# Kernel tuning notes

Measured on AMD Instinct MI355X. Metric: run time of the kernel, lower is better.

Reference implementation:

```python
import jax, jax.numpy as jnp
import numpy as np

N, E, F, H, C, G = 100000, 800000, 128, 128, 10, 128
EPS = 1e-5


def setup_inputs() -> dict:
    key = jax.random.key(0)
    ks = jax.random.split(key, 8)
    return {
        "x": jax.random.normal(ks[0], (N, F), jnp.float32),
        "edge_index": jax.random.randint(ks[1], (2, E), 0, N),
        "batch": jnp.sort(jax.random.randint(ks[2], (N,), 0, G)),
        "edge_weight": jax.random.uniform(ks[3], (E,), jnp.float32, 0.1, 1.0),
        "bn_feat_w": jnp.ones((F,), jnp.float32),
        "bn_feat_b": jnp.full((F,), 1e-4, jnp.float32),
        "conv_feat_W": jax.random.normal(ks[4], (F, H), jnp.float32) / np.float32(np.sqrt(F)),
        "conv_feat_b": jnp.zeros((H,), jnp.float32),
        "bns_w": jnp.ones((3, H), jnp.float32),
        "bns_b": jnp.full((3, H), 1e-4, jnp.float32),
        "convs_W": jax.random.normal(ks[5], (3, H, H), jnp.float32) / np.float32(np.sqrt(H)),
        "convs_b": jnp.zeros((3, H), jnp.float32),
        "bn_fc_w": jnp.ones((H,), jnp.float32),
        "bn_fc_b": jnp.full((H,), 1e-4, jnp.float32),
        "lin_fc_W": jax.random.normal(ks[6], (H, H), jnp.float32) / np.float32(np.sqrt(H)),
        "lin_fc_b": jnp.zeros((H,), jnp.float32),
        "bn_hidden_w": jnp.ones((H,), jnp.float32),
        "bn_hidden_b": jnp.full((H,), 1e-4, jnp.float32),
        "lin_class_W": jax.random.normal(ks[7], (H, C), jnp.float32) / np.float32(np.sqrt(H)),
        "lin_class_b": jnp.zeros((C,), jnp.float32),
    }


def _bn(h, w, b):
    # training-mode BatchNorm1d: biased batch stats over dim 0
    mu = h.mean(0)
    var = jnp.mean((h - mu) ** 2, 0)
    return (h - mu) * jax.lax.rsqrt(var + EPS) * w + b


def reference(x, edge_index, batch, edge_weight,
              bn_feat_w, bn_feat_b, conv_feat_W, conv_feat_b,
              bns_w, bns_b, convs_W, convs_b,
              bn_fc_w, bn_fc_b, lin_fc_W, lin_fc_b,
              bn_hidden_w, bn_hidden_b, lin_class_W, lin_class_b):
    n = x.shape[0]
    loops = jnp.arange(n)
    # PyG GCNConv: add self-loops (weight 1) + symmetric normalization, shared by all convs
    row = jnp.concatenate([edge_index[0], loops])
    col = jnp.concatenate([edge_index[1], loops])
    ew = jnp.concatenate([edge_weight, jnp.ones((n,), x.dtype)])
    deg = jax.ops.segment_sum(ew, col, num_segments=n)
    dinv = jnp.where(deg > 0, jax.lax.rsqrt(jnp.maximum(deg, EPS)), 0.0)
    norm = (dinv[row] * ew * dinv[col])[:, None]  # [E+N, 1]

    def conv(h, W, b):
        m = (h @ W)[row] * norm                 # gather + scale per edge
        return jax.ops.segment_sum(m, col, num_segments=n) + b

    h = _bn(x, bn_feat_w, bn_feat_b)
    h = jax.nn.relu(conv(h, conv_feat_W, conv_feat_b))
    h_init = h

    x_list = []
    # branch 1: BN -> Conv -> ReLU chain
    h = h_init
    for i in range(3):
        h = jax.nn.relu(conv(_bn(h, bns_w[i], bns_b[i]), convs_W[i], convs_b[i]))
    x_list.append(h)
    # branch 2: double application of the same BN/Conv per step
    h = h_init
    for i in range(3):
        h_ = jax.nn.relu(conv(_bn(h, bns_w[i], bns_b[i]), convs_W[i], convs_b[i]))
        h = jax.nn.relu(conv(_bn(h_, bns_w[i], bns_b[i]), convs_W[i], convs_b[i]))
    x_list.append(h)
    # branch 3: identical to branch 1 when conv_residual=False
    h = h_init
    for i in range(3):
        h = jax.nn.relu(conv(_bn(h, bns_w[i], bns_b[i]), convs_W[i], convs_b[i]))
    x_list.append(h)
    # branch 4: BN -> ReLU only
    h = h_init
    for i in range(3):
        h = jax.nn.relu(_bn(h, bns_w[i], bns_b[i]))
    x_list.append(h)

    def head(hn):
        g = jax.ops.segment_sum(hn, batch, num_segments=G)  # global_add_pool
        g = jax.nn.relu(_bn(g, bn_fc_w, bn_fc_b) @ lin_fc_W + lin_fc_b)
        g = _bn(g, bn_hidden_w, bn_hidden_b)
        return jax.nn.log_softmax(g @ lin_class_W + lin_class_b, axis=-1)

    return tuple(head(hn) for hn in x_list)
```

## Files before the change

kernel.cpp:

```cpp
#include <hip/hip_runtime.h>

#define N_NODES 100000
#define NPAD    100032
#define NBLK    1563
#define NEDGE   800000
#define NGRP    128
#define NSLOT   32
#define EPS     1e-5f

typedef unsigned int   u32;
typedef unsigned short u16;
typedef short bf16x8 __attribute__((ext_vector_type(8)));
typedef float f32x4  __attribute__((ext_vector_type(4)));

__device__ __forceinline__ float bf2f(u32 u){ return __uint_as_float(u << 16); }
__device__ __forceinline__ u16 f2bf(float f){
  u32 x = __float_as_uint(f);
  x += 0x7fffu + ((x >> 16) & 1u);
  return (u16)(x >> 16);
}

__global__ void k_init(float* deg, int* cnt, int* fill, float* gbuf){
  int i = blockIdx.x * 256 + threadIdx.x;
  if (i < NPAD){ deg[i] = 1.0f; cnt[i] = 0; fill[i] = 0; }
  if (i < 4 * NGRP * 128) gbuf[i] = 0.f;
}

__global__ void k_deg(const int* __restrict__ col, const float* __restrict__ ew,
                      float* __restrict__ deg, int* __restrict__ cnt){
  int e = blockIdx.x * 256 + threadIdx.x;
  if (e < NEDGE){
    int c = col[e];
    atomicAdd(&deg[c], ew[e]);
    atomicAdd(&cnt[c], 1);
  }
}

__global__ void k_dinv(const float* __restrict__ deg, float* __restrict__ dinv, float* __restrict__ srow){
  int i = blockIdx.x * 256 + threadIdx.x;
  if (i < N_NODES){
    float d = deg[i];
    float v = d > 0.f ? rsqrtf(fmaxf(d, EPS)) : 0.f;
    dinv[i] = v; srow[i] = v * v;
  }
}

__global__ __launch_bounds__(256) void k_chunksum(const int* __restrict__ cnt, int* __restrict__ csum){
  int b = blockIdx.x, t = threadIdx.x;
  int s = 0;
  for (int i = t; i < 1024; i += 256){ int idx = b * 1024 + i; if (idx < N_NODES) s += cnt[idx]; }
  __shared__ int red[256];
  red[t] = s; __syncthreads();
  for (int o = 128; o > 0; o >>= 1){ if (t < o) red[t] += red[t + o]; __syncthreads(); }
  if (t == 0) csum[b] = red[0];
}

__global__ __launch_bounds__(128) void k_chunkscan(const int* __restrict__ csum, int* __restrict__ coff,
                                                   int* __restrict__ ptrA){
  int t = threadIdx.x;
  __shared__ int s[128];
  int v = (t < 98) ? csum[t] : 0;
  s[t] = v; __syncthreads();
  for (int o = 1; o < 128; o <<= 1){
    int x = (t >= o) ? s[t - o] : 0;
    __syncthreads(); s[t] += x; __syncthreads();
  }
  if (t < 98) coff[t] = s[t] - v;
  if (t == 0) ptrA[N_NODES] = NEDGE;
}

__global__ __launch_bounds__(256) void k_scan2(const int* __restrict__ cnt, const int* __restrict__ coff,
                                               int* __restrict__ ptrA){
  int b = blockIdx.x, t = threadIdx.x;
  int base = b * 1024 + t * 4;
  int v[4], tot = 0;
  #pragma unroll
  for (int k = 0; k < 4; k++){ int idx = base + k; v[k] = (idx < N_NODES) ? cnt[idx] : 0; tot += v[k]; }
  __shared__ int sc[256];
  sc[t] = tot; __syncthreads();
  for (int o = 1; o < 256; o <<= 1){
    int x = (t >= o) ? sc[t - o] : 0;
    __syncthreads(); sc[t] += x; __syncthreads();
  }
  int off = coff[b] + sc[t] - tot;
  #pragma unroll
  for (int k = 0; k < 4; k++){ int idx = base + k; if (idx < N_NODES) ptrA[idx] = off; off += v[k]; }
}

__global__ void k_fill(const int* __restrict__ row, const int* __restrict__ col,
                       const float* __restrict__ ew, const float* __restrict__ dinv,
                       const int* __restrict__ ptrA, int* __restrict__ fill, int2* __restrict__ adj,
                       float* __restrict__ srow){
  int e = blockIdx.x * 256 + threadIdx.x;
  if (e < NEDGE){
    int r = row[e], c = col[e];
    float w = dinv[r] * ew[e] * dinv[c];
    int pos = ptrA[c] + atomicAdd(&fill[c], 1);
    adj[pos] = make_int2(r, __float_as_int(w));
    atomicAdd(&srow[c], w);
  }
}

__global__ __launch_bounds__(256) void k_bhist(const int* __restrict__ batch, int* __restrict__ bpart){
  __shared__ int loc[128];
  int t = threadIdx.x;
  if (t < 128) loc[t] = 0;
  __syncthreads();
  int i = blockIdx.x * 256 + t;
  if (i < N_NODES) atomicAdd(&loc[batch[i]], 1);
  __syncthreads();
  if (t < 128) bpart[blockIdx.x * 128 + t] = loc[t];
}

__global__ __launch_bounds__(128) void k_bscan(const int* __restrict__ bpart, int* __restrict__ gptr){
  int t = threadIdx.x;
  int v = 0;
  for (int p = 0; p < 391; p++) v += bpart[p * 128 + t];
  __shared__ int s[128];
  s[t] = v; __syncthreads();
  for (int o = 1; o < 128; o <<= 1){
    int x = (t >= o) ? s[t - o] : 0;
    __syncthreads(); s[t] += x; __syncthreads();
  }
  gptr[t + 1] = s[t];
  if (t == 0) gptr[0] = 0;
}

__global__ __launch_bounds__(256) void k_cvtstats(const float* __restrict__ x, u32* __restrict__ dst,
                                                  float* __restrict__ sums_out){
  __shared__ float R[1024];
  int t = threadIdx.x;
  float s0 = 0.f, q0 = 0.f, s1 = 0.f, q1 = 0.f;
  size_t base = (size_t)blockIdx.x * 4096 + t;
  #pragma unroll
  for (int it = 0; it < 16; it++){
    size_t idx = base + (size_t)it * 256;
    if (idx < (size_t)N_NODES * 64){
      float2 v = ((const float2*)x)[idx];
      dst[idx] = (u32)f2bf(v.x) | ((u32)f2bf(v.y) << 16);
      s0 += v.x; q0 += v.x * v.x; s1 += v.y; q1 += v.y * v.y;
    }
  }
  R[t] = s0; R[256 + t] = q0; R[512 + t] = s1; R[768 + t] = q1;
  __syncthreads();
  if (t < 64){
    float S0 = 0.f, Q0 = 0.f, S1 = 0.f, Q1 = 0.f;
    #pragma unroll
    for (int g = 0; g < 4; g++){
      S0 += R[g * 64 + t];       Q0 += R[256 + g * 64 + t];
      S1 += R[512 + g * 64 + t]; Q1 += R[768 + g * 64 + t];
    }
    float* so = sums_out + (blockIdx.x & (NSLOT - 1)) * 256;
    atomicAdd(&so[2 * t], S0);
    atomicAdd(&so[2 * t + 1], S1);
    atomicAdd(&so[128 + 2 * t], Q0);
    atomicAdd(&so[128 + 2 * t + 1], Q1);
  }
}

__global__ __launch_bounds__(1024) void k_fold(const float* __restrict__ sums,
    const float* __restrict__ bw, const float* __restrict__ bb,
    const float* __restrict__ W, const float* __restrict__ bias,
    u16* __restrict__ Wh, u16* __restrict__ Wl, float* __restrict__ rb){
  __shared__ float scl[128], shf[128], rbs[128], stot[256];
  int t = threadIdx.x;
  if (t < 256){
    float s = 0.f;
    #pragma unroll 4
    for (int sl = 0; sl < NSLOT; sl++) s += sums[sl * 256 + t];
    stot[t] = s;
  } else if (t < 384) rbs[t - 256] = 0.f;
  __syncthreads();
  if (t < 128){
    float mu  = stot[t] * (1.f / N_NODES);
    float var = stot[128 + t] * (1.f / N_NODES) - mu * mu;
    float sc  = bw[t] * rsqrtf(var + EPS);
    scl[t] = sc; shf[t] = bb[t] - mu * sc;
  }
  __syncthreads();
  #pragma unroll
  for (int r = 0; r < 2; r++){
    int idx = r * 1024 + t;
    int lane_ = idx & 63, sl = idx >> 6;
    int nt_ = sl >> 2, ks_ = sl & 3;
    int n_ = nt_ * 16 + (lane_ & 15);
    int kb = ks_ * 32 + (lane_ >> 4) * 8;
    float rp = 0.f;
    u16 hi8[8], lo8[8];
    #pragma unroll
    for (int j = 0; j < 8; j++){
      float wv = W[(kb + j) * 128 + n_];
      rp += shf[kb + j] * wv;
      float xv = scl[kb + j] * wv;
      u16 hh = f2bf(xv);
      hi8[j] = hh; lo8[j] = f2bf(xv - bf2f(hh));
    }
    uint4 ph, pl;
    ph.x = (u32)hi8[0] | ((u32)hi8[1] << 16); ph.y = (u32)hi8[2] | ((u32)hi8[3] << 16);
    ph.z = (u32)hi8[4] | ((u32)hi8[5] << 16); ph.w = (u32)hi8[6] | ((u32)hi8[7] << 16);
    pl.x = (u32)lo8[0] | ((u32)lo8[1] << 16); pl.y = (u32)lo8[2] | ((u32)lo8[3] << 16);
    pl.z = (u32)lo8[4] | ((u32)lo8[5] << 16); pl.w = (u32)lo8[6] | ((u32)lo8[7] << 16);
    *(uint4*)&Wh[idx * 8] = ph;
    *(uint4*)&Wl[idx * 8] = pl;
    atomicAdd(&rbs[n_], rp);
  }
  __syncthreads();
  if (t < 128){
    rb[t] = rbs[t];
    rb[128 + t] = bias[t];
  }
}

#define CONV_EPILOGUE(RB, HOUT, SOUT)                                          \
  __syncthreads();                                                             \
  sred[t] = 0.f;                                                               \
  __syncthreads();                                                             \
  _Pragma("unroll")                                                            \
  for (int nt = 0; nt < 8; nt++){                                              \
    int colc = nt * 16 + m;                                                    \
    float rv = RB[colc], bv = RB[128 + colc];                                  \
    float s = 0.f, qq = 0.f;                                                   \
    _Pragma("unroll")                                                          \
    for (int r = 0; r < 4; r++){                                               \
      int rown = row0 + q * 4 + r;                                             \
      float v = C[nt][r] + srow[rown] * rv + bv;                               \
      v = fmaxf(v, 0.f);                                                       \
      u16 sv = f2bf(v);                                                        \
      HOUT[(size_t)rown * 128 + colc] = sv;                                    \
      if (rown < N_NODES){ float vv = bf2f(sv); s += vv; qq += vv * vv; }      \
    }                                                                          \
    atomicAdd(&sred[colc], s);                                                 \
    atomicAdd(&sred[128 + colc], qq);                                          \
  }                                                                            \
  __syncthreads();                                                             \
  atomicAdd(&SOUT[(blockIdx.x & (NSLOT - 1)) * 256 + t], sred[t]);

#define GATHER_PHASE()                                                         \
  _Pragma("unroll")                                                            \
  for (int ks = 0; ks < 4; ks++)                                               \
    _Pragma("unroll")                                                          \
    for (int j = 0; j < 8; j++) acc[ks][j] = 0.f;                              \
  if (i < N_NODES){                                                            \
    const u16* hq = h + q * 8;                                                 \
    float di = dinv[i], sw = di * di;                                          \
    _Pragma("unroll")                                                          \
    for (int ks = 0; ks < 4; ks++){                                            \
      uint4 v = *(const uint4*)(hq + (size_t)i * 128 + ks * 32);               \
      acc[ks][0] = sw * __uint_as_float(v.x << 16); acc[ks][1] = sw * __uint_as_float(v.x & 0xffff0000u); \
      acc[ks][2] = sw * __uint_as_float(v.y << 16); acc[ks][3] = sw * __uint_as_float(v.y & 0xffff0000u); \
      acc[ks][4] = sw * __uint_as_float(v.z << 16); acc[ks][5] = sw * __uint_as_float(v.z & 0xffff0000u); \
      acc[ks][6] = sw * __uint_as_float(v.w << 16); acc[ks][7] = sw * __uint_as_float(v.w & 0xffff0000u); \
    }                                                                          \
    int b = ptrA[i], e = ptrA[i + 1];                                          \
    int k = b;                                                                 \
    for (; k + 2 <= e; k += 2){                                                \
      int2 a0 = adj[k], a1 = adj[k + 1];                                       \
      const u16* r0p = hq + (size_t)a0.x * 128;                                \
      const u16* r1p = hq + (size_t)a1.x * 128;                                \
      uint4 u0 = *(const uint4*)(r0p);                                         \
      uint4 u1 = *(const uint4*)(r0p + 32);                                    \
      uint4 u2 = *(const uint4*)(r0p + 64);                                    \
      uint4 u3 = *(const uint4*)(r0p + 96);                                    \
      uint4 w0 = *(const uint4*)(r1p);                                         \
      uint4 w1 = *(const uint4*)(r1p + 32);                                    \
      uint4 w2 = *(const uint4*)(r1p + 64);                                    \
      uint4 w3 = *(const uint4*)(r1p + 96);                                    \
      float f0 = __int_as_float(a0.y), f1 = __int_as_float(a1.y);              \
      FMA_KS(0, u0, f0) FMA_KS(1, u1, f0) FMA_KS(2, u2, f0) FMA_KS(3, u3, f0)  \
      FMA_KS(0, w0, f1) FMA_KS(1, w1, f1) FMA_KS(2, w2, f1) FMA_KS(3, w3, f1)  \
    }                                                                          \
    for (; k < e; k++){                                                        \
      int2 a0 = adj[k];                                                        \
      const u16* r0p = hq + (size_t)a0.x * 128;                                \
      uint4 u0 = *(const uint4*)(r0p);                                         \
      uint4 u1 = *(const uint4*)(r0p + 32);                                    \
      uint4 u2 = *(const uint4*)(r0p + 64);                                    \
      uint4 u3 = *(const uint4*)(r0p + 96);                                    \
      float f0 = __int_as_float(a0.y);                                         \
      FMA_KS(0, u0, f0) FMA_KS(1, u1, f0) FMA_KS(2, u2, f0) FMA_KS(3, u3, f0)  \
    }                                                                          \
  }

#define FMA_KS(KS, V, WT) \
  acc[KS][0] += (WT) * __uint_as_float((V).x << 16); acc[KS][1] += (WT) * __uint_as_float((V).x & 0xffff0000u); \
  acc[KS][2] += (WT) * __uint_as_float((V).y << 16); acc[KS][3] += (WT) * __uint_as_float((V).y & 0xffff0000u); \
  acc[KS][4] += (WT) * __uint_as_float((V).z << 16); acc[KS][5] += (WT) * __uint_as_float((V).z & 0xffff0000u); \
  acc[KS][6] += (WT) * __uint_as_float((V).w << 16); acc[KS][7] += (WT) * __uint_as_float((V).w & 0xffff0000u);

#define MFMA_3PASS(WH, WL_)                                                    \
  _Pragma("unroll")                                                            \
  for (int ks = 0; ks < 4; ks++){                                              \
    _Pragma("unroll")                                                          \
    for (int nt = 0; nt < 8; nt++){                                            \
      bf16x8 bh = ((const bf16x8*)WH)[(nt * 4 + ks) * 64 + lane];              \
      bf16x8 bl = ((const bf16x8*)WL_)[(nt * 4 + ks) * 64 + lane];             \
      C[nt] = __builtin_amdgcn_mfma_f32_16x16x32_bf16(AH[ks], bh, C[nt], 0, 0, 0); \
      C[nt] = __builtin_amdgcn_mfma_f32_16x16x32_bf16(AL[ks], bh, C[nt], 0, 0, 0); \
      C[nt] = __builtin_amdgcn_mfma_f32_16x16x32_bf16(AH[ks], bl, C[nt], 0, 0, 0); \
    }                                                                          \
  }

__global__ __launch_bounds__(256, 4) void k_conv(
    const u16* __restrict__ h, const int* __restrict__ ptrA, const int2* __restrict__ adj,
    const float* __restrict__ dinv, const float* __restrict__ srow,
    const u16* __restrict__ Wh, const u16* __restrict__ Wl, const float* __restrict__ rb,
    u16* __restrict__ hout, float* __restrict__ sums_out){
  __shared__ float sred[256];
  int t = threadIdx.x;
  int wave = t >> 6, lane = t & 63, m = lane & 15, q = lane >> 4;
  int row0 = blockIdx.x * 64 + wave * 16;
  int i = row0 + m;
  float acc[4][8];
  GATHER_PHASE()
  bf16x8 AH[4], AL[4];
  #pragma unroll
  for (int ks = 0; ks < 4; ks++)
    #pragma unroll
    for (int j = 0; j < 8; j++){
      u16 hh = f2bf(acc[ks][j]);
      AH[ks][j] = (short)hh;
      AL[ks][j] = (short)f2bf(acc[ks][j] - bf2f(hh));
    }
  f32x4 C[8];
  #pragma unroll
  for (int nt = 0; nt < 8; nt++) C[nt] = f32x4{0.f, 0.f, 0.f, 0.f};
  MFMA_3PASS(Wh, Wl)
  CONV_EPILOGUE(rb, hout, sums_out)
}

__global__ __launch_bounds__(256, 4) void k_dualconv(
    const u16* __restrict__ h, const int* __restrict__ ptrA, const int2* __restrict__ adj,
    const float* __restrict__ dinv, const float* __restrict__ srow,
    const u16* __restrict__ Wh1, const u16* __restrict__ Wl1, const float* __restrict__ rb1,
    u16* __restrict__ hout1, float* __restrict__ sums1,
    const u16* __restrict__ Wh2, const u16* __restrict__ Wl2, const float* __restrict__ rb2,
    u16* __restrict__ hout2, float* __restrict__ sums2){
  __shared__ float sred[256];
  int t = threadIdx.x;
  int wave = t >> 6, lane = t & 63, m = lane & 15, q = lane >> 4;
  int row0 = blockIdx.x * 64 + wave * 16;
  int i = row0 + m;
  float acc[4][8];
  GATHER_PHASE()
  bf16x8 AH[4], AL[4];
  #pragma unroll
  for (int ks = 0; ks < 4; ks++)
    #pragma unroll
    for (int j = 0; j < 8; j++){
      u16 hh = f2bf(acc[ks][j]);
      AH[ks][j] = (short)hh;
      AL[ks][j] = (short)f2bf(acc[ks][j] - bf2f(hh));
    }
  f32x4 C[8];
  #pragma unroll
  for (int nt = 0; nt < 8; nt++) C[nt] = f32x4{0.f, 0.f, 0.f, 0.f};
  MFMA_3PASS(Wh1, Wl1)
  CONV_EPILOGUE(rb1, hout1, sums1)
  #pragma unroll
  for (int nt = 0; nt < 8; nt++) C[nt] = f32x4{0.f, 0.f, 0.f, 0.f};
  MFMA_3PASS(Wh2, Wl2)
  CONV_EPILOGUE(rb2, hout2, sums2)
}

__global__ __launch_bounds__(256) void k_normrelu(const u16* __restrict__ h, const float* __restrict__ sums,
    const float* __restrict__ bw, const float* __restrict__ bb, u16* __restrict__ o,
    float* __restrict__ sums_out){
  __shared__ float scl[128], shf[128], R[1024], stot[256];
  int t = threadIdx.x;
  {
    float s = 0.f;
    #pragma unroll 4
    for (int sl = 0; sl < NSLOT; sl++) s += sums[sl * 256 + t];
    stot[t] = s;
  }
  __syncthreads();
  if (t < 128){
    float mu  = stot[t] * (1.f / N_NODES);
    float var = stot[128 + t] * (1.f / N_NODES) - mu * mu;
    float sc  = bw[t] * rsqrtf(var + EPS);
    scl[t] = sc; shf[t] = bb[t] - mu * sc;
  }
  __syncthreads();
  int c0 = (t & 63) * 2;
  float sc0 = scl[c0], sh0 = shf[c0], sc1 = scl[c0 + 1], sh1 = shf[c0 + 1];
  float s0 = 0.f, q0 = 0.f, s1 = 0.f, q1 = 0.f;
  size_t base = (size_t)blockIdx.x * 4096 + t;
  #pragma unroll
  for (int it = 0; it < 16; it++){
    size_t idx = base + (size_t)it * 256;
    if (idx < (size_t)N_NODES * 64){
      u32 v = ((const u32*)h)[idx];
      float x0 = fmaxf(bf2f(v & 0xffffu) * sc0 + sh0, 0.f);
      float x1 = fmaxf(bf2f(v >> 16) * sc1 + sh1, 0.f);
      u16 r0 = f2bf(x0), r1 = f2bf(x1);
      ((u32*)o)[idx] = (u32)r0 | ((u32)r1 << 16);
      float y0 = bf2f(r0), y1 = bf2f(r1);
      s0 += y0; q0 += y0 * y0; s1 += y1; q1 += y1 * y1;
    }
  }
  R[t] = s0; R[256 + t] = q0; R[512 + t] = s1; R[768 + t] = q1;
  __syncthreads();
  if (t < 64){
    float S0 = 0.f, Q0 = 0.f, S1 = 0.f, Q1 = 0.f;
    #pragma unroll
    for (int g = 0; g < 4; g++){
      S0 += R[g * 64 + t];       Q0 += R[256 + g * 64 + t];
      S1 += R[512 + g * 64 + t]; Q1 += R[768 + g * 64 + t];
    }
    float* so = sums_out + (blockIdx.x & (NSLOT - 1)) * 256;
    atomicAdd(&so[2 * t], S0);
    atomicAdd(&so[2 * t + 1], S1);
    atomicAdd(&so[128 + 2 * t], Q0);
    atomicAdd(&so[128 + 2 * t + 1], Q1);
  }
}

__global__ __launch_bounds__(128) void k_pool(const u16* __restrict__ h, const int* __restrict__ gptr,
                                              float* __restrict__ gdst){
  int g = blockIdx.x >> 3, s = blockIdx.x & 7, t = threadIdx.x;
  int b = gptr[g], e = gptr[g + 1];
  int len = e - b, per = (len + 7) >> 3;
  int r0 = b + s * per, r1 = min(r0 + per, e);
  float acc = 0.f;
  for (int r = r0; r < r1; r++) acc += bf2f(h[(size_t)r * 128 + t]);
  atomicAdd(&gdst[g * 128 + t], acc);
}

__global__ __launch_bounds__(256) void k_head(const float* __restrict__ gbuf,
    const float* __restrict__ fcw, const float* __restrict__ fcb,
    const float* __restrict__ Wfc, const float* __restrict__ bfc,
    const float* __restrict__ bhw, const float* __restrict__ bhb,
    const float* __restrict__ Wcl, const float* __restrict__ bcl,
    float* __restrict__ out){
  __shared__ float GS[128 * 65];
  __shared__ float ls[256], lq[256];
  __shared__ float scl[128], shf[128], scl2[128], shf2[128];
  __shared__ float sumT[128], sumQ[128];
  __shared__ float WclT[1280], Lrow[1280];
  int t = threadIdx.x, br = blockIdx.x;
  int slot = (br == 1) ? 1 : (br == 3 ? 3 : 0);
  const float* G = gbuf + slot * 16384;
  {
    int col = t & 127, hf2 = t >> 7;
    float s = 0.f, q = 0.f;
    for (int g = hf2 * 64; g < hf2 * 64 + 64; g++){ float v = G[g * 128 + col]; s += v; q += v * v; }
    ls[t] = s; lq[t] = q;
  }
  for (int idx = t; idx < 1280; idx += 256){
    int cc = idx >> 7, c = idx & 127;
    WclT[idx] = Wcl[c * 10 + cc];
  }
  if (t < 128){ sumT[t] = 0.f; sumQ[t] = 0.f; }
  __syncthreads();
  if (t < 128){
    float s = ls[t] + ls[t + 128], q = lq[t] + lq[t + 128];
    float mu = s * (1.f / 128), var = q * (1.f / 128) - mu * mu;
    float sc = fcw[t] * rsqrtf(var + EPS);
    scl[t] = sc; shf[t] = fcb[t] - mu * sc;
  }
  __syncthreads();
  int tr = t >> 4, tc = t & 15, r0 = tr * 8, c0 = tc * 8;
  float acc[8][8];
  #pragma unroll
  for (int a = 0; a < 8; a++)
    #pragma unroll
    for (int b = 0; b < 8; b++) acc[a][b] = 0.f;
  for (int kh = 0; kh < 2; kh++){
    for (int idx = t; idx < 8192; idx += 256){
      int r = idx >> 6, kk = idx & 63, f = kh * 64 + kk;
      GS[r * 65 + kk] = G[r * 128 + f] * scl[f] + shf[f];
    }
    __syncthreads();
    #pragma unroll 2
    for (int k = 0; k < 64; k++){
      float a[8];
      #pragma unroll
      for (int ri = 0; ri < 8; ri++) a[ri] = GS[(r0 + ri) * 65 + k];
      float4 b0 = *(const float4*)&Wfc[(kh * 64 + k) * 128 + c0];
      float4 b1 = *(const float4*)&Wfc[(kh * 64 + k) * 128 + c0 + 4];
      float bb[8] = {b0.x, b0.y, b0.z, b0.w, b1.x, b1.y, b1.z, b1.w};
      #pragma unroll
      for (int ri = 0; ri < 8; ri++)
        #pragma unroll
        for (int ci = 0; ci < 8; ci++) acc[ri][ci] += a[ri] * bb[ci];
    }
    __syncthreads();
  }
  #pragma unroll
  for (int ci = 0; ci < 8; ci++){
    float bb = bfc[c0 + ci];
    float s = 0.f, q = 0.f;
    #pragma unroll
    for (int ri = 0; ri < 8; ri++){
      float v = fmaxf(acc[ri][ci] + bb, 0.f);
      acc[ri][ci] = v; s += v; q += v * v;
    }
    atomicAdd(&sumT[c0 + ci], s);
    atomicAdd(&sumQ[c0 + ci], q);
  }
  __syncthreads();
  if (t < 128){
    float mu = sumT[t] * (1.f / 128), var = sumQ[t] * (1.f / 128) - mu * mu;
    float sc = bhw[t] * rsqrtf(var + EPS);
    scl2[t] = sc; shf2[t] = bhb[t] - mu * sc;
  }
  __syncthreads();
  #pragma unroll
  for (int ci = 0; ci < 8; ci++){
    float sc = scl2[c0 + ci], sh = shf2[c0 + ci];
    #pragma unroll
    for (int ri = 0; ri < 8; ri++) acc[ri][ci] = acc[ri][ci] * sc + sh;
  }
  #pragma unroll
  for (int ri = 0; ri < 8; ri++){
    float pl[10];
    #pragma unroll
    for (int cc = 0; cc < 10; cc++) pl[cc] = 0.f;
    #pragma unroll
    for (int ci = 0; ci < 8; ci++){
      float v = acc[ri][ci];
      #pragma unroll
      for (int cc = 0; cc < 10; cc++) pl[cc] += v * WclT[cc * 128 + c0 + ci];
    }
    #pragma unroll
    for (int msk = 1; msk < 16; msk <<= 1)
      #pragma unroll
      for (int cc = 0; cc < 10; cc++) pl[cc] += __shfl_xor(pl[cc], msk, 64);
    if (tc == 0)
      #pragma unroll
      for (int cc = 0; cc < 10; cc++) Lrow[(r0 + ri) * 10 + cc] = pl[cc];
  }
  __syncthreads();
  if (t < 128){
    float l[10];
    #pragma unroll
    for (int cc = 0; cc < 10; cc++) l[cc] = Lrow[t * 10 + cc] + bcl[cc];
    float m = l[0];
    #pragma unroll
    for (int cc = 1; cc < 10; cc++) m = fmaxf(m, l[cc]);
    float se = 0.f;
    #pragma unroll
    for (int cc = 0; cc < 10; cc++) se += expf(l[cc] - m);
    float lse = m + logf(se);
    #pragma unroll
    for (int cc = 0; cc < 10; cc++) out[br * 1280 + t * 10 + cc] = l[cc] - lse;
  }
}

extern "C" void kernel_launch(void* const* d_in, const int* in_sizes, int n_in,
                              void* d_out, int out_size, void* d_ws, size_t ws_size,
                              hipStream_t stream){
  const float* x    = (const float*)d_in[0];
  const int*  ei    = (const int*)d_in[1];
  const int*  batch = (const int*)d_in[2];
  const float* ew   = (const float*)d_in[3];
  const float* bnfw = (const float*)d_in[4];
  const float* bnfb = (const float*)d_in[5];
  const float* cfW  = (const float*)d_in[6];
  const float* cfb  = (const float*)d_in[7];
  const float* bnsw = (const float*)d_in[8];
  const float* bnsb = (const float*)d_in[9];
  const float* cvW  = (const float*)d_in[10];
  const float* cvb  = (const float*)d_in[11];
  const float* fcw  = (const float*)d_in[12];
  const float* fcb  = (const float*)d_in[13];
  const float* Wfc  = (const float*)d_in[14];
  const float* bfc  = (const float*)d_in[15];
  const float* bhw  = (const float*)d_in[16];
  const float* bhb  = (const float*)d_in[17];
  const float* Wcl  = (const float*)d_in[18];
  const float* bcl  = (const float*)d_in[19];
  float* out = (float*)d_out;

  char* p = (char*)d_ws;
  auto carve = [&](size_t bytes)->void*{ void* r = (void*)p; p += (bytes + 255) & ~(size_t)255; return r; };
  float* deg  = (float*)carve((size_t)NPAD * 4);
  float* dinv = (float*)carve((size_t)NPAD * 4);
  float* srow = (float*)carve((size_t)NPAD * 4);
  int*   cnt  = (int*)carve((size_t)NPAD * 4);
  int*   fill = (int*)carve((size_t)NPAD * 4);
  int*   ptrA = (int*)carve((size_t)(NPAD + 1) * 4);
  int*   bpart= (int*)carve((size_t)391 * 128 * 4);
  int*   csum = (int*)carve(512);
  int*   coff = (int*)carve(512);
  int*   gptr = (int*)carve(1024);
  float* S    = (float*)carve((size_t)13 * NSLOT * 1024);
  float* gbuf = (float*)carve(4 * 128 * 128 * 4);
  u16*   F0h  = (u16*)carve(32768);  u16* F0l = (u16*)carve(32768);  float* F0r = (float*)carve(1024);
  u16*   F1h  = (u16*)carve(32768);  u16* F1l = (u16*)carve(32768);  float* F1r = (float*)carve(1024);
  u16*   F2h  = (u16*)carve(32768);  u16* F2l = (u16*)carve(32768);  float* F2r = (float*)carve(1024);
  u16*   B0   = (u16*)carve((size_t)NPAD * 256);
  u16*   B1   = (u16*)carve((size_t)NPAD * 256);
  u16*   B2   = (u16*)carve((size_t)NPAD * 256);
  u16*   B3   = (u16*)carve((size_t)NPAD * 256);
  int2*  adj  = (int2*)carve((size_t)NEDGE * 8);
  u16*   Xb   = B3;
  auto Sb = [&](int i){ return S + (size_t)i * NSLOT * 256; };

  (void)hipMemsetAsync(S, 0, (size_t)13 * NSLOT * 1024, stream);

  k_init<<<392, 256, 0, stream>>>(deg, cnt, fill, gbuf);
  k_deg<<<3125, 256, 0, stream>>>(ei + NEDGE, ew, deg, cnt);
  k_dinv<<<391, 256, 0, stream>>>(deg, dinv, srow);
  k_chunksum<<<98, 256, 0, stream>>>(cnt, csum);
  k_chunkscan<<<1, 128, 0, stream>>>(csum, coff, ptrA);
  k_scan2<<<98, 256, 0, stream>>>(cnt, coff, ptrA);
  k_fill<<<3125, 256, 0, stream>>>(ei, ei + NEDGE, ew, dinv, ptrA, fill, adj, srow);
  k_bhist<<<391, 256, 0, stream>>>(batch, bpart);
  k_bscan<<<1, 128, 0, stream>>>(bpart, gptr);
  k_cvtstats<<<NBLK, 256, 0, stream>>>(x, (u32*)Xb, Sb(0));

  auto fold = [&](const float* Sin, const float* bw, const float* bb,
                  const float* W, const float* bias, u16* Fh, u16* Fl, float* Fr){
    k_fold<<<1, 1024, 0, stream>>>(Sin, bw, bb, W, bias, Fh, Fl, Fr);
  };
  auto conv = [&](const u16* hin, const u16* Fh, const u16* Fl, const float* Fr,
                  u16* hout, float* Sout){
    k_conv<<<NBLK, 256, 0, stream>>>(hin, ptrA, adj, dinv, srow, Fh, Fl, Fr, hout, Sout);
  };

  fold(Sb(0), bnfw, bnfb, cfW, cfb, F0h, F0l, F0r);
  conv(Xb, F0h, F0l, F0r, B0, Sb(1));
  fold(Sb(1), bnsw, bnsb, cvW, cvb, F1h, F1l, F1r);
  conv(B0, F1h, F1l, F1r, B1, Sb(2));
  k_normrelu<<<NBLK, 256, 0, stream>>>(B0, Sb(1), bnsw,       bnsb,       B2, Sb(3));
  k_normrelu<<<NBLK, 256, 0, stream>>>(B2, Sb(3), bnsw + 128, bnsb + 128, B3, Sb(4));
  k_normrelu<<<NBLK, 256, 0, stream>>>(B3, Sb(4), bnsw + 256, bnsb + 256, B2, Sb(12));
  k_pool<<<1024, 128, 0, stream>>>(B2, gptr, gbuf + 3 * 16384);
  fold(Sb(2), bnsw + 128, bnsb + 128, cvW + 16384, cvb + 128, F0h, F0l, F0r);
  fold(Sb(2), bnsw,       bnsb,       cvW,         cvb,       F1h, F1l, F1r);
  k_dualconv<<<NBLK, 256, 0, stream>>>(B1, ptrA, adj, dinv, srow,
      F0h, F0l, F0r, B3, Sb(5),
      F1h, F1l, F1r, B2, Sb(6));
  fold(Sb(5), bnsw + 256, bnsb + 256, cvW + 32768, cvb + 256, F2h, F2l, F2r);
  conv(B3, F2h, F2l, F2r, B0, Sb(10));
  k_pool<<<1024, 128, 0, stream>>>(B0, gptr, gbuf);
  fold(Sb(6), bnsw + 128, bnsb + 128, cvW + 16384, cvb + 128, F0h, F0l, F0r);
  conv(B2, F0h, F0l, F0r, B1, Sb(7));
  fold(Sb(7), bnsw + 128, bnsb + 128, cvW + 16384, cvb + 128, F1h, F1l, F1r);
  conv(B1, F1h, F1l, F1r, B2, Sb(8));
  fold(Sb(8), bnsw + 256, bnsb + 256, cvW + 32768, cvb + 256, F2h, F2l, F2r);
  conv(B2, F2h, F2l, F2r, B1, Sb(9));
  fold(Sb(9), bnsw + 256, bnsb + 256, cvW + 32768, cvb + 256, F0h, F0l, F0r);
  conv(B1, F0h, F0l, F0r, B3, Sb(11));
  k_pool<<<1024, 128, 0, stream>>>(B3, gptr, gbuf + 16384);

  k_head<<<4, 256, 0, stream>>>(gbuf, fcw, fcb, Wfc, bfc, bhw, bhb, Wcl, bcl, out);
}
```

Measured before the change: 1.201 ms.

## Merge independent convs into one launch, parallelize fold, unroll gather by four

Adds k_conv2, which runs two independent GCN convs (branch 1 last layer and branch 2 step) in a single grid of twice the blocks, removing a launch and a serialization point. k_fold is split across 8 blocks of 256 threads, with a shared-memory tree reduction replacing the LDS atomics for the bias term. The conv epilogue reduces column stats across quads with wave shuffles before the LDS atomics. The gather loop is unrolled to 4 edges per iteration, and launch bounds drop to 3 blocks per CU, trading occupancy for more loads in flight and more registers.

After: 1.109 ms. 7.7% less time.

```diff
diff --git a/kernel.cpp b/kernel.cpp
--- a/kernel.cpp
+++ b/kernel.cpp
@@ -158,18 +158,18 @@
   }
 }
 
-__global__ __launch_bounds__(1024) void k_fold(const float* __restrict__ sums,
+__global__ __launch_bounds__(256) void k_fold(const float* __restrict__ sums,
     const float* __restrict__ bw, const float* __restrict__ bb,
     const float* __restrict__ W, const float* __restrict__ bias,
     u16* __restrict__ Wh, u16* __restrict__ Wl, float* __restrict__ rb){
-  __shared__ float scl[128], shf[128], rbs[128], stot[256];
-  int t = threadIdx.x;
-  if (t < 256){
+  __shared__ float scl[128], shf[128], stot[256], rred[256];
+  int t = threadIdx.x, blk = blockIdx.x;
+  {
     float s = 0.f;
     #pragma unroll 4
     for (int sl = 0; sl < NSLOT; sl++) s += sums[sl * 256 + t];
     stot[t] = s;
-  } else if (t < 384) rbs[t - 256] = 0.f;
+  }
   __syncthreads();
   if (t < 128){
     float mu  = stot[t] * (1.f / N_NODES);
@@ -178,19 +178,16 @@
     scl[t] = sc; shf[t] = bb[t] - mu * sc;
   }
   __syncthreads();
-  #pragma unroll
-  for (int r = 0; r < 2; r++){
-    int idx = r * 1024 + t;
+  {
+    int idx = blk * 256 + t;
     int lane_ = idx & 63, sl = idx >> 6;
     int nt_ = sl >> 2, ks_ = sl & 3;
     int n_ = nt_ * 16 + (lane_ & 15);
     int kb = ks_ * 32 + (lane_ >> 4) * 8;
-    float rp = 0.f;
     u16 hi8[8], lo8[8];
     #pragma unroll
     for (int j = 0; j < 8; j++){
       float wv = W[(kb + j) * 128 + n_];
-      rp += shf[kb + j] * wv;
       float xv = scl[kb + j] * wv;
       u16 hh = f2bf(xv);
       hi8[j] = hh; lo8[j] = f2bf(xv - bf2f(hh));
@@ -202,16 +199,30 @@
     pl.z = (u32)lo8[4] | ((u32)lo8[5] << 16); pl.w = (u32)lo8[6] | ((u32)lo8[7] << 16);
     *(uint4*)&Wh[idx * 8] = ph;
     *(uint4*)&Wl[idx * 8] = pl;
-    atomicAdd(&rbs[n_], rp);
-  }
-  __syncthreads();
-  if (t < 128){
-    rb[t] = rbs[t];
-    rb[128 + t] = bias[t];
-  }
-}
-
-#define CONV_EPILOGUE(RB, HOUT, SOUT)                                          \
+  }
+  {
+    int nl = t & 15, kk = t >> 4;
+    int n2 = blk * 16 + nl;
+    float rp = 0.f;
+    #pragma unroll
+    for (int j = 0; j < 8; j++){
+      int k2 = kk * 8 + j;
+      rp += shf[k2] * W[k2 * 128 + n2];
+    }
+    rred[t] = rp;
+  }
+  __syncthreads();
+  if (t < 16){
+    float s = 0.f;
+    #pragma unroll
+    for (int kk2 = 0; kk2 < 16; kk2++) s += rred[kk2 * 16 + t];
+    int n2 = blk * 16 + t;
+    rb[n2] = s;
+    rb[128 + n2] = bias[n2];
+  }
+}
+
+#define CONV_EPILOGUE(RB, HOUT, SOUT, BLK)                                     \
   __syncthreads();                                                             \
   sred[t] = 0.f;                                                               \
   __syncthreads();                                                             \
@@ -229,11 +240,15 @@
       HOUT[(size_t)rown * 128 + colc] = sv;                                    \
       if (rown < N_NODES){ float vv = bf2f(sv); s += vv; qq += vv * vv; }      \
     }                                                                          \
-    atomicAdd(&sred[colc], s);                                                 \
-    atomicAdd(&sred[128 + colc], qq);                                          \
+    s  += __shfl_xor(s, 16, 64);  s  += __shfl_xor(s, 32, 64);                 \
+    qq += __shfl_xor(qq, 16, 64); qq += __shfl_xor(qq, 32, 64);                \
+    if (q == 0){                                                               \
+      atomicAdd(&sred[colc], s);                                               \
+      atomicAdd(&sred[128 + colc], qq);                                        \
+    }                                                                          \
   }                                                                            \
   __syncthreads();                                                             \
-  atomicAdd(&SOUT[(blockIdx.x & (NSLOT - 1)) * 256 + t], sred[t]);
+  atomicAdd(&SOUT[((BLK) & (NSLOT - 1)) * 256 + t], sred[t]);
 
 #define GATHER_PHASE()                                                         \
   _Pragma("unroll")                                                            \
@@ -253,6 +268,27 @@
     }                                                                          \
     int b = ptrA[i], e = ptrA[i + 1];                                          \
     int k = b;                                                                 \
+    for (; k + 4 <= e; k += 4){                                                \
+      int2 a0 = adj[k], a1 = adj[k + 1], a2 = adj[k + 2], a3 = adj[k + 3];     \
+      const u16* p0 = hq + (size_t)a0.x * 128;                                 \
+      const u16* p1 = hq + (size_t)a1.x * 128;                                 \
+      const u16* p2 = hq + (size_t)a2.x * 128;                                 \
+      const u16* p3 = hq + (size_t)a3.x * 128;                                 \
+      uint4 u0 = *(const uint4*)(p0);      uint4 u1 = *(const uint4*)(p0 + 32);\
+      uint4 u2 = *(const uint4*)(p0 + 64); uint4 u3 = *(const uint4*)(p0 + 96);\
+      uint4 v0 = *(const uint4*)(p1);      uint4 v1 = *(const uint4*)(p1 + 32);\
+      uint4 v2 = *(const uint4*)(p1 + 64); uint4 v3 = *(const uint4*)(p1 + 96);\
+      uint4 w0 = *(const uint4*)(p2);      uint4 w1 = *(const uint4*)(p2 + 32);\
+      uint4 w2 = *(const uint4*)(p2 + 64); uint4 w3 = *(const uint4*)(p2 + 96);\
+      uint4 y0 = *(const uint4*)(p3);      uint4 y1 = *(const uint4*)(p3 + 32);\
+      uint4 y2 = *(const uint4*)(p3 + 64); uint4 y3 = *(const uint4*)(p3 + 96);\
+      float f0 = __int_as_float(a0.y), f1 = __int_as_float(a1.y);              \
+      float f2 = __int_as_float(a2.y), f3 = __int_as_float(a3.y);              \
+      FMA_KS(0, u0, f0) FMA_KS(1, u1, f0) FMA_KS(2, u2, f0) FMA_KS(3, u3, f0)  \
+      FMA_KS(0, v0, f1) FMA_KS(1, v1, f1) FMA_KS(2, v2, f1) FMA_KS(3, v3, f1)  \
+      FMA_KS(0, w0, f2) FMA_KS(1, w1, f2) FMA_KS(2, w2, f2) FMA_KS(3, w3, f2)  \
+      FMA_KS(0, y0, f3) FMA_KS(1, y1, f3) FMA_KS(2, y2, f3) FMA_KS(3, y3, f3)  \
+    }                                                                          \
     for (; k + 2 <= e; k += 2){                                                \
       int2 a0 = adj[k], a1 = adj[k + 1];                                       \
       const u16* r0p = hq + (size_t)a0.x * 128;                                \
@@ -269,7 +305,7 @@
       FMA_KS(0, u0, f0) FMA_KS(1, u1, f0) FMA_KS(2, u2, f0) FMA_KS(3, u3, f0)  \
       FMA_KS(0, w0, f1) FMA_KS(1, w1, f1) FMA_KS(2, w2, f1) FMA_KS(3, w3, f1)  \
     }                                                                          \
-    for (; k < e; k++){                                                        \
+    if (k < e){                                                                \
       int2 a0 = adj[k];                                                        \
       const u16* r0p = hq + (size_t)a0.x * 128;                                \
       uint4 u0 = *(const uint4*)(r0p);                                         \
@@ -286,6 +322,17 @@
   acc[KS][2] += (WT) * __uint_as_float((V).y << 16); acc[KS][3] += (WT) * __uint_as_float((V).y & 0xffff0000u); \
   acc[KS][4] += (WT) * __uint_as_float((V).z << 16); acc[KS][5] += (WT) * __uint_as_float((V).z & 0xffff0000u); \
   acc[KS][6] += (WT) * __uint_as_float((V).w << 16); acc[KS][7] += (WT) * __uint_as_float((V).w & 0xffff0000u);
+
+#define BUILD_AFRAG()                                                          \
+  bf16x8 AH[4], AL[4];                                                         \
+  _Pragma("unroll")                                                            \
+  for (int ks = 0; ks < 4; ks++)                                               \
+    _Pragma("unroll")                                                          \
+    for (int j = 0; j < 8; j++){                                               \
+      u16 hh = f2bf(acc[ks][j]);                                               \
+      AH[ks][j] = (short)hh;                                                   \
+      AL[ks][j] = (short)f2bf(acc[ks][j] - bf2f(hh));                          \
+    }
 
 #define MFMA_3PASS(WH, WL_)                                                    \
   _Pragma("unroll")                                                            \
@@ -300,7 +347,7 @@
     }                                                                          \
   }
 
-__global__ __launch_bounds__(256, 4) void k_conv(
+__global__ __launch_bounds__(256, 3) void k_conv(
     const u16* __restrict__ h, const int* __restrict__ ptrA, const int2* __restrict__ adj,
     const float* __restrict__ dinv, const float* __restrict__ srow,
     const u16* __restrict__ Wh, const u16* __restrict__ Wl, const float* __restrict__ rb,
@@ -308,27 +355,52 @@
   __shared__ float sred[256];
   int t = threadIdx.x;
   int wave = t >> 6, lane = t & 63, m = lane & 15, q = lane >> 4;
-  int row0 = blockIdx.x * 64 + wave * 16;
+  int blk = blockIdx.x;
+  int row0 = blk * 64 + wave * 16;
   int i = row0 + m;
   float acc[4][8];
   GATHER_PHASE()
-  bf16x8 AH[4], AL[4];
-  #pragma unroll
-  for (int ks = 0; ks < 4; ks++)
-    #pragma unroll
-    for (int j = 0; j < 8; j++){
-      u16 hh = f2bf(acc[ks][j]);
-      AH[ks][j] = (short)hh;
-      AL[ks][j] = (short)f2bf(acc[ks][j] - bf2f(hh));
-    }
+  BUILD_AFRAG()
   f32x4 C[8];
   #pragma unroll
   for (int nt = 0; nt < 8; nt++) C[nt] = f32x4{0.f, 0.f, 0.f, 0.f};
   MFMA_3PASS(Wh, Wl)
-  CONV_EPILOGUE(rb, hout, sums_out)
-}
-
-__global__ __launch_bounds__(256, 4) void k_dualconv(
+  CONV_EPILOGUE(rb, hout, sums_out, blk)
+}
+
+__global__ __launch_bounds__(256, 3) void k_conv2(
+    const u16* __restrict__ hA, const u16* __restrict__ hB,
+    const int* __restrict__ ptrA, const int2* __restrict__ adj,
+    const float* __restrict__ dinv, const float* __restrict__ srow,
+    const u16* __restrict__ WhA, const u16* __restrict__ WlA, const float* __restrict__ rbA,
+    u16* __restrict__ houtA, float* __restrict__ sumsA,
+    const u16* __restrict__ WhB, const u16* __restrict__ WlB, const float* __restrict__ rbB,
+    u16* __restrict__ houtB, float* __restrict__ sumsB){
+  __shared__ float sred[256];
+  int t = threadIdx.x;
+  int wave = t >> 6, lane = t & 63, m = lane & 15, q = lane >> 4;
+  int bb = blockIdx.x;
+  int second = bb >= NBLK;
+  int blk = second ? bb - NBLK : bb;
+  const u16* h = second ? hB : hA;
+  const u16* Wh = second ? WhB : WhA;
+  const u16* Wl = second ? WlB : WlA;
+  const float* rb = second ? rbB : rbA;
+  u16* hout = second ? houtB : houtA;
+  float* sums_out = second ? sumsB : sumsA;
+  int row0 = blk * 64 + wave * 16;
+  int i = row0 + m;
+  float acc[4][8];
+  GATHER_PHASE()
+  BUILD_AFRAG()
+  f32x4 C[8];
+  #pragma unroll
+  for (int nt = 0; nt < 8; nt++) C[nt] = f32x4{0.f, 0.f, 0.f, 0.f};
+  MFMA_3PASS(Wh, Wl)
+  CONV_EPILOGUE(rb, hout, sums_out, blk)
+}
+
+__global__ __launch_bounds__(256, 3) void k_dualconv(
     const u16* __restrict__ h, const int* __restrict__ ptrA, const int2* __restrict__ adj,
     const float* __restrict__ dinv, const float* __restrict__ srow,
     const u16* __restrict__ Wh1, const u16* __restrict__ Wl1, const float* __restrict__ rb1,
@@ -338,28 +410,21 @@
   __shared__ float sred[256];
   int t = threadIdx.x;
   int wave = t >> 6, lane = t & 63, m = lane & 15, q = lane >> 4;
-  int row0 = blockIdx.x * 64 + wave * 16;
+  int blk = blockIdx.x;
+  int row0 = blk * 64 + wave * 16;
   int i = row0 + m;
   float acc[4][8];
   GATHER_PHASE()
-  bf16x8 AH[4], AL[4];
-  #pragma unroll
-  for (int ks = 0; ks < 4; ks++)
-    #pragma unroll
-    for (int j = 0; j < 8; j++){
-      u16 hh = f2bf(acc[ks][j]);
-      AH[ks][j] = (short)hh;
-      AL[ks][j] = (short)f2bf(acc[ks][j] - bf2f(hh));
-    }
+  BUILD_AFRAG()
   f32x4 C[8];
   #pragma unroll
   for (int nt = 0; nt < 8; nt++) C[nt] = f32x4{0.f, 0.f, 0.f, 0.f};
   MFMA_3PASS(Wh1, Wl1)
-  CONV_EPILOGUE(rb1, hout1, sums1)
+  CONV_EPILOGUE(rb1, hout1, sums1, blk)
   #pragma unroll
   for (int nt = 0; nt < 8; nt++) C[nt] = f32x4{0.f, 0.f, 0.f, 0.f};
   MFMA_3PASS(Wh2, Wl2)
-  CONV_EPILOGUE(rb2, hout2, sums2)
+  CONV_EPILOGUE(rb2, hout2, sums2, blk)
 }
 
 __global__ __launch_bounds__(256) void k_normrelu(const u16* __restrict__ h, const float* __restrict__ sums,
@@ -612,7 +677,7 @@
 
   auto fold = [&](const float* Sin, const float* bw, const float* bb,
                   const float* W, const float* bias, u16* Fh, u16* Fl, float* Fr){
-    k_fold<<<1, 1024, 0, stream>>>(Sin, bw, bb, W, bias, Fh, Fl, Fr);
+    k_fold<<<8, 256, 0, stream>>>(Sin, bw, bb, W, bias, Fh, Fl, Fr);
   };
   auto conv = [&](const u16* hin, const u16* Fh, const u16* Fl, const float* Fr,
                   u16* hout, float* Sout){
@@ -633,10 +698,11 @@
       F0h, F0l, F0r, B3, Sb(5),
       F1h, F1l, F1r, B2, Sb(6));
   fold(Sb(5), bnsw + 256, bnsb + 256, cvW + 32768, cvb + 256, F2h, F2l, F2r);
-  conv(B3, F2h, F2l, F2r, B0, Sb(10));
+  fold(Sb(6), bnsw + 128, bnsb + 128, cvW + 16384, cvb + 128, F0h, F0l, F0r);
+  k_conv2<<<2 * NBLK, 256, 0, stream>>>(B3, B2, ptrA, adj, dinv, srow,
+      F2h, F2l, F2r, B0, Sb(10),
+      F0h, F0l, F0r, B1, Sb(7));
   k_pool<<<1024, 128, 0, stream>>>(B0, gptr, gbuf);
-  fold(Sb(6), bnsw + 128, bnsb + 128, cvW + 16384, cvb + 128, F0h, F0l, F0r);
-  conv(B2, F0h, F0l, F0r, B1, Sb(7));
   fold(Sb(7), bnsw + 128, bnsb + 128, cvW + 16384, cvb + 128, F1h, F1l, F1r);
   conv(B1, F1h, F1l, F1r, B2, Sb(8));
   fold(Sb(8), bnsw + 256, bnsb + 256, cvW + 32768, cvb + 256, F2h, F2l, F2r);
```
